# Optimization experiments

Hardware: AMD Instinct MI355X
Metric: run time of the kernel (lower is better)

## Reference

```python
import jax, jax.numpy as jnp
import numpy as np

DIM = 128
NUM_HEADS = 4
HEAD_DIM = DIM // NUM_HEADS
KSIZE = 7
DILATION = 1
SCALE = HEAD_DIM ** -0.5


def _rpb_bias(rpb):
    # Faithful to _get_rpb_indices: indices do NOT depend on query position.
    coords = np.stack(np.meshgrid(np.arange(KSIZE), np.arange(KSIZE), indexing='ij'))
    coords = coords.reshape(2, -1).T  # [K*K, 2]
    rel = coords - KSIZE // 2 + (KSIZE - 1)
    return rpb[:, rel[:, 0], rel[:, 1]]  # [NH, K*K]


def setup_inputs() -> dict:
    key = jax.random.key(0)
    ks = jax.random.split(key, 6)
    B, H, W = 4, 56, 56
    x = jax.random.normal(ks[0], (B, H, W, DIM), dtype=jnp.float32)
    qkv_w = jax.random.normal(ks[1], (3 * DIM, DIM), dtype=jnp.float32) * 0.02
    qkv_b = jnp.zeros((3 * DIM,), dtype=jnp.float32)
    rpb = jax.random.normal(ks[2], (NUM_HEADS, 2 * KSIZE - 1, 2 * KSIZE - 1), dtype=jnp.float32) * 0.02
    proj_w = jax.random.normal(ks[3], (DIM, DIM), dtype=jnp.float32) * 0.02
    proj_b = jnp.zeros((DIM,), dtype=jnp.float32)
    return {"x": x, "qkv_w": qkv_w, "qkv_b": qkv_b, "rpb": rpb, "proj_w": proj_w, "proj_b": proj_b}


def reference(x, qkv_w, qkv_b, rpb, proj_w, proj_b):
    B, H, W, C = x.shape
    qkv = x @ qkv_w.T + qkv_b                                   # [B,H,W,3C]
    qkv = qkv.reshape(B, H, W, 3, NUM_HEADS, HEAD_DIM).transpose(3, 0, 4, 1, 2, 5)
    q, k, v = qkv[0], qkv[1], qkv[2]                            # [B,NH,H,W,HD]

    pad = (KSIZE // 2) * DILATION
    # Zero padding — padded positions stay in the softmax (faithful, no masking).
    kp = jnp.pad(k, ((0, 0), (0, 0), (pad, pad), (pad, pad), (0, 0)))
    vp = jnp.pad(v, ((0, 0), (0, 0), (pad, pad), (pad, pad), (0, 0)))

    off = jnp.arange(0, KSIZE * DILATION, DILATION)
    idx_i = jnp.arange(H)[:, None] + off[None, :]               # [H,K]
    idx_j = jnp.arange(W)[:, None] + off[None, :]               # [W,K]
    Ai = idx_i[:, None, :, None]                                # [H,1,K,1]
    Aj = idx_j[None, :, None, :]                                # [1,W,1,K]
    k_win = kp[:, :, Ai, Aj, :].reshape(B, NUM_HEADS, H, W, KSIZE * KSIZE, HEAD_DIM)
    v_win = vp[:, :, Ai, Aj, :].reshape(B, NUM_HEADS, H, W, KSIZE * KSIZE, HEAD_DIM)

    bias = _rpb_bias(rpb)                                       # [NH, K*K]
    attn = jnp.einsum('bnhwd,bnhwkd->bnhwk', q, k_win) * SCALE
    attn = attn + bias[None, :, None, None, :]
    attn = jax.nn.softmax(attn, axis=-1)
    out = jnp.einsum('bnhwk,bnhwkd->bnhwd', attn, v_win)        # [B,NH,H,W,HD]
    out = out.transpose(0, 2, 3, 1, 4).reshape(B, H, W, C)
    return out @ proj_w.T + proj_b
```

## Files before the change

kernel.cpp:

```cpp
#include <hip/hip_runtime.h>

#define NPIX   3136
#define MROWS  12544
#define QKV_STRIDE 1605632
#define SCALE  0.17677669529663687f
#define KVS    136
#define HP     140

typedef __attribute__((ext_vector_type(8))) _Float16 half8;
typedef __attribute__((ext_vector_type(2))) _Float16 v2h;
typedef __attribute__((ext_vector_type(4))) float    f32x4;

#if defined(__has_builtin)
#if __has_builtin(__builtin_amdgcn_fdot2)
#define HAS_FDOT2 1
#endif
#endif

__device__ __forceinline__ float quad_reduce_sum(float x) {
    x += __int_as_float(__builtin_amdgcn_mov_dpp(__float_as_int(x), 0xB1, 0xF, 0xF, true));
    x += __int_as_float(__builtin_amdgcn_mov_dpp(__float_as_int(x), 0x4E, 0xF, 0xF, true));
    return x;
}

__device__ __forceinline__ float dot8h(half8 a, half8 b, float acc) {
#ifdef HAS_FDOT2
    union { half8 v; v2h p[4]; } ua, ub;
    ua.v = a; ub.v = b;
    acc = __builtin_amdgcn_fdot2(ua.p[0], ub.p[0], acc, false);
    acc = __builtin_amdgcn_fdot2(ua.p[1], ub.p[1], acc, false);
    acc = __builtin_amdgcn_fdot2(ua.p[2], ub.p[2], acc, false);
    acc = __builtin_amdgcn_fdot2(ua.p[3], ub.p[3], acc, false);
#else
#pragma unroll
    for (int i = 0; i < 8; ++i) acc += (float)a[i] * (float)b[i];
#endif
    return acc;
}

template<int BM, int BN, int WM, int WN>
__global__ __launch_bounds__(256)
void qkv_mfma(const float* __restrict__ A, const float* __restrict__ W,
              const float* __restrict__ bias, _Float16* __restrict__ outh,
              const float* __restrict__ pw, _Float16* __restrict__ pwh)
{
    constexpr int WTM = BM / WM;
    constexpr int WTN = BN / WN;
    constexpr int FM  = WTM / 16;
    constexpr int FN  = WTN / 16;
    constexpr int AIT = BM * 16 / 256;
    constexpr int WIT = BN * 16 / 256;
    const int row0 = blockIdx.x * BM;
    const int col0 = blockIdx.y * BN;
    const int t  = threadIdx.x;
    const int w  = t >> 6;
    const int l  = t & 63;
    const int wm = w / WN;
    const int wn = w % WN;

    if (blockIdx.y == 0 && blockIdx.x < 16) {
        int idx = blockIdx.x * 256 + t;
        float4 v = *reinterpret_cast<const float4*>(pw + (size_t)idx * 4);
        union { _Float16 h[4]; uint2 u; } cv;
        cv.h[0] = (_Float16)v.x; cv.h[1] = (_Float16)v.y;
        cv.h[2] = (_Float16)v.z; cv.h[3] = (_Float16)v.w;
        *reinterpret_cast<uint2*>(pwh + (size_t)idx * 4) = cv.u;
    }

    __shared__ _Float16 Ah[BM * 128];
    __shared__ _Float16 Wh[BN * 128];

    float4 pa[AIT], pwr[WIT];

#pragma unroll
    for (int it = 0; it < AIT; ++it) {
        int idx = t + it * 256;
        int r = idx >> 4, k0 = (idx & 15) << 2;
        pa[it] = *reinterpret_cast<const float4*>(A + (size_t)(row0 + r) * 128 + k0);
    }
#pragma unroll
    for (int it = 0; it < WIT; ++it) {
        int idx = t + it * 256;
        int r = idx >> 4, k0 = (idx & 15) << 2;
        pwr[it] = *reinterpret_cast<const float4*>(W + (size_t)(col0 + r) * 128 + k0);
    }
#pragma unroll
    for (int it = 0; it < AIT; ++it) {
        int idx = t + it * 256;
        int r = idx >> 4, k0 = (idx & 15) << 2;
        union { _Float16 h[4]; uint2 u; } cv;
        cv.h[0] = (_Float16)pa[it].x; cv.h[1] = (_Float16)pa[it].y;
        cv.h[2] = (_Float16)pa[it].z; cv.h[3] = (_Float16)pa[it].w;
        *reinterpret_cast<uint2*>(&Ah[r * 128 + (k0 ^ ((r & 7) << 3))]) = cv.u;
    }
#pragma unroll
    for (int it = 0; it < WIT; ++it) {
        int idx = t + it * 256;
        int r = idx >> 4, k0 = (idx & 15) << 2;
        union { _Float16 h[4]; uint2 u; } cv;
        cv.h[0] = (_Float16)pwr[it].x; cv.h[1] = (_Float16)pwr[it].y;
        cv.h[2] = (_Float16)pwr[it].z; cv.h[3] = (_Float16)pwr[it].w;
        *reinterpret_cast<uint2*>(&Wh[r * 128 + (k0 ^ ((r & 7) << 3))]) = cv.u;
    }
    __syncthreads();

#pragma unroll
    for (int it = 0; it < AIT; ++it) {
        int idx = t + it * 256;
        int r = idx >> 4, k0 = 64 + ((idx & 15) << 2);
        pa[it] = *reinterpret_cast<const float4*>(A + (size_t)(row0 + r) * 128 + k0);
    }
#pragma unroll
    for (int it = 0; it < WIT; ++it) {
        int idx = t + it * 256;
        int r = idx >> 4, k0 = 64 + ((idx & 15) << 2);
        pwr[it] = *reinterpret_cast<const float4*>(W + (size_t)(col0 + r) * 128 + k0);
    }

    f32x4 acc[FM][FN];
#pragma unroll
    for (int mf = 0; mf < FM; ++mf)
#pragma unroll
        for (int nf = 0; nf < FN; ++nf) acc[mf][nf] = (f32x4){0.f, 0.f, 0.f, 0.f};

#pragma unroll
    for (int ks = 0; ks < 2; ++ks) {
        const int kb = ks * 32 + ((l >> 4) << 3);
        half8 a[FM], b[FN];
#pragma unroll
        for (int mf = 0; mf < FM; ++mf) {
            int m = wm * WTM + mf * 16 + (l & 15);
            a[mf] = *reinterpret_cast<const half8*>(&Ah[m * 128 + (kb ^ ((m & 7) << 3))]);
        }
#pragma unroll
        for (int nf = 0; nf < FN; ++nf) {
            int n = wn * WTN + nf * 16 + (l & 15);
            b[nf] = *reinterpret_cast<const half8*>(&Wh[n * 128 + (kb ^ ((n & 7) << 3))]);
        }
#pragma unroll
        for (int mf = 0; mf < FM; ++mf)
#pragma unroll
            for (int nf = 0; nf < FN; ++nf)
                acc[mf][nf] = __builtin_amdgcn_mfma_f32_16x16x32_f16(
                    a[mf], b[nf], acc[mf][nf], 0, 0, 0);
    }

#pragma unroll
    for (int it = 0; it < AIT; ++it) {
        int idx = t + it * 256;
        int r = idx >> 4, k0 = 64 + ((idx & 15) << 2);
        union { _Float16 h[4]; uint2 u; } cv;
        cv.h[0] = (_Float16)pa[it].x; cv.h[1] = (_Float16)pa[it].y;
        cv.h[2] = (_Float16)pa[it].z; cv.h[3] = (_Float16)pa[it].w;
        *reinterpret_cast<uint2*>(&Ah[r * 128 + (k0 ^ ((r & 7) << 3))]) = cv.u;
    }
#pragma unroll
    for (int it = 0; it < WIT; ++it) {
        int idx = t + it * 256;
        int r = idx >> 4, k0 = 64 + ((idx & 15) << 2);
        union { _Float16 h[4]; uint2 u; } cv;
        cv.h[0] = (_Float16)pwr[it].x; cv.h[1] = (_Float16)pwr[it].y;
        cv.h[2] = (_Float16)pwr[it].z; cv.h[3] = (_Float16)pwr[it].w;
        *reinterpret_cast<uint2*>(&Wh[r * 128 + (k0 ^ ((r & 7) << 3))]) = cv.u;
    }
    __syncthreads();

#pragma unroll
    for (int ks = 2; ks < 4; ++ks) {
        const int kb = ks * 32 + ((l >> 4) << 3);
        half8 a[FM], b[FN];
#pragma unroll
        for (int mf = 0; mf < FM; ++mf) {
            int m = wm * WTM + mf * 16 + (l & 15);
            a[mf] = *reinterpret_cast<const half8*>(&Ah[m * 128 + (kb ^ ((m & 7) << 3))]);
        }
#pragma unroll
        for (int nf = 0; nf < FN; ++nf) {
            int n = wn * WTN + nf * 16 + (l & 15);
            b[nf] = *reinterpret_cast<const half8*>(&Wh[n * 128 + (kb ^ ((n & 7) << 3))]);
        }
#pragma unroll
        for (int mf = 0; mf < FM; ++mf)
#pragma unroll
            for (int nf = 0; nf < FN; ++nf)
                acc[mf][nf] = __builtin_amdgcn_mfma_f32_16x16x32_f16(
                    a[mf], b[nf], acc[mf][nf], 0, 0, 0);
    }

#pragma unroll
    for (int mf = 0; mf < FM; ++mf) {
#pragma unroll
        for (int nf = 0; nf < FN; ++nf) {
#pragma unroll
            for (int r = 0; r < 4; ++r) {
                int row = row0 + wm * WTM + mf * 16 + ((l >> 4) << 2) + r;
                int col = col0 + wn * WTN + nf * 16 + (l & 15);
                float val = acc[mf][nf][r] + bias[col];
                int b_  = row / NPIX;
                int pix = row - b_ * NPIX;
                int which = col >> 7;
                outh[(size_t)which * QKV_STRIDE +
                     ((size_t)b_ * NPIX + pix) * 128 + (col & 127)] = (_Float16)val;
            }
        }
    }
}

__global__ __launch_bounds__(512, 4)
void natten_proj_k(const _Float16* __restrict__ qb, const _Float16* __restrict__ kb,
                   const _Float16* __restrict__ vb, const float* __restrict__ rpb,
                   const _Float16* __restrict__ pwh, const float* __restrict__ pb,
                   float* __restrict__ out)
{
    extern __shared__ _Float16 smem[];
    _Float16* ksm  = smem;
    _Float16* vsm  = smem + HP * KVS;
    _Float16* atts = smem;

    const int flat = blockIdx.x;
    const int rank = (flat & 7) * 49 + (flat >> 3);
    const int tile = rank % 98;
    const int b    = rank / 98;
    const int ti = (tile / 14) * 8;
    const int tj = (tile % 14) * 4;
    const int t   = threadIdx.x;
    const int sub = t & 3;
    const int px  = (t >> 2) & 31;
    const int pi  = px >> 2;
    const int pj  = px & 3;
    const int h   = t >> 7;

    const _Float16* kbase = kb + (size_t)b * NPIX * 128;
    const _Float16* vbase = vb + (size_t)b * NPIX * 128;

    const int pix = (ti + pi) * 56 + (tj + pj);
    half8 qv = *reinterpret_cast<const half8*>(
        qb + ((size_t)b * NPIX + pix) * 128 + h * 32 + sub * 8);

    for (int e = t; e < HP * 16; e += 512) {
        int p = e >> 4, g = e & 15;
        int wi = p / 10, wj = p - wi * 10;
        int gi = ti - 3 + wi, gj = tj - 3 + wj;
        bool ok = ((unsigned)gi < 56u) && ((unsigned)gj < 56u);
        size_t src = ((size_t)(gi * 56 + gj)) * 128 + g * 8;
        half8 kv = (half8){0,0,0,0,0,0,0,0};
        if (ok) kv = *reinterpret_cast<const half8*>(kbase + src);
        *reinterpret_cast<half8*>(&ksm[p * KVS + g * 8]) = kv;
        half8 vv = (half8){0,0,0,0,0,0,0,0};
        if (ok) vv = *reinterpret_cast<const half8*>(vbase + src);
        *reinterpret_cast<half8*>(&vsm[p * KVS + g * 8]) = vv;
    }

    __syncthreads();

    const float* bias = rpb + h * 169;
    float logits[49];
    float m = -1e30f;
#pragma unroll
    for (int ki = 0; ki < 7; ++ki) {
#pragma unroll
        for (int kj = 0; kj < 7; ++kj) {
            int nb = (pi + ki) * 10 + (pj + kj);
            half8 kk = *reinterpret_cast<const half8*>(&ksm[nb * KVS + h * 32 + sub * 8]);
            float s = dot8h(qv, kk, 0.f);
            s = quad_reduce_sum(s);
            float lg = s * SCALE + bias[(ki + 3) * 13 + (kj + 3)];
            logits[ki * 7 + kj] = lg;
            m = fmaxf(m, lg);
        }
    }

    __syncthreads();

    float sum = 0.f;
#pragma unroll
    for (int n = 0; n < 49; ++n) {
        float e = __expf(logits[n] - m);
        logits[n] = e;
        sum += e;
    }
    float inv = 1.f / sum;

    float o[8] = {0.f, 0.f, 0.f, 0.f, 0.f, 0.f, 0.f, 0.f};
#pragma unroll
    for (int ki = 0; ki < 7; ++ki) {
#pragma unroll
        for (int kj = 0; kj < 7; ++kj) {
            int nb = (pi + ki) * 10 + (pj + kj);
            half8 vv = *reinterpret_cast<const half8*>(&vsm[nb * KVS + h * 32 + sub * 8]);
            float wgt = logits[ki * 7 + kj];
#pragma unroll
            for (int i = 0; i < 8; ++i)
                o[i] += wgt * (float)vv[i];
        }
    }

    const int l   = t & 63;
    const int wv  = t >> 6;
    const int wm  = wv & 1;
    const int wn  = wv >> 1;
    const int kb0 = (l >> 4) << 3;
    half8 wreg[8];
#pragma unroll
    for (int ks = 0; ks < 4; ++ks) {
        const _Float16* wp = pwh + (size_t)(wn * 32 + (l & 15)) * 128 + ks * 32 + kb0;
        wreg[ks]     = *reinterpret_cast<const half8*>(wp);
        wreg[4 + ks] = *reinterpret_cast<const half8*>(wp + 16 * 128);
    }

    {
        half8 r;
#pragma unroll
        for (int i = 0; i < 8; ++i) r[i] = (_Float16)(o[i] * inv);
        *reinterpret_cast<half8*>(&atts[px * KVS + h * 32 + sub * 8]) = r;
    }

    __syncthreads();

    f32x4 acc0 = (f32x4){0.f, 0.f, 0.f, 0.f};
    f32x4 acc1 = (f32x4){0.f, 0.f, 0.f, 0.f};
#pragma unroll
    for (int ks = 0; ks < 4; ++ks) {
        const int kb = ks * 32 + kb0;
        half8 a = *reinterpret_cast<const half8*>(&atts[(wm * 16 + (l & 15)) * KVS + kb]);
        acc0 = __builtin_amdgcn_mfma_f32_16x16x32_f16(a, wreg[ks],     acc0, 0, 0, 0);
        acc1 = __builtin_amdgcn_mfma_f32_16x16x32_f16(a, wreg[4 + ks], acc1, 0, 0, 0);
    }

#pragma unroll
    for (int r = 0; r < 4; ++r) {
        int prow = wm * 16 + ((l >> 4) << 2) + r;
        int gpix = (ti + (prow >> 2)) * 56 + tj + (prow & 3);
        float* dst = out + ((size_t)b * NPIX + gpix) * 128;
        int c0 = wn * 32 + (l & 15);
        dst[c0]      = acc0[r] + pb[c0];
        dst[c0 + 16] = acc1[r] + pb[c0 + 16];
    }
}

extern "C" void kernel_launch(void* const* d_in, const int* in_sizes, int n_in,
                              void* d_out, int out_size, void* d_ws, size_t ws_size,
                              hipStream_t stream)
{
    const float* x      = (const float*)d_in[0];
    const float* qkv_w  = (const float*)d_in[1];
    const float* qkv_b  = (const float*)d_in[2];
    const float* rpb    = (const float*)d_in[3];
    const float* proj_w = (const float*)d_in[4];
    const float* proj_b = (const float*)d_in[5];
    float* out = (float*)d_out;

    _Float16* qbuf = (_Float16*)d_ws;
    _Float16* kbuf = qbuf + (size_t)QKV_STRIDE;
    _Float16* vbuf = kbuf + (size_t)QKV_STRIDE;
    _Float16* pwh  = vbuf + (size_t)QKV_STRIDE;

    hipFuncSetAttribute((const void*)natten_proj_k,
                        hipFuncAttributeMaxDynamicSharedMemorySize,
                        2 * HP * KVS * (int)sizeof(_Float16));

    qkv_mfma<64, 128, 2, 2><<<dim3(196, 3), dim3(256), 0, stream>>>(
        x, qkv_w, qkv_b, qbuf, proj_w, pwh);

    natten_proj_k<<<dim3(392), dim3(512),
                    2 * HP * KVS * sizeof(_Float16), stream>>>(
        qbuf, kbuf, vbuf, rpb, pwh, proj_b, out);
}
```

Measured before the change: 30.41 us.

## Shrink attention tiles to 4x4 with XOR-swizzled K/V shared memory

The fused attention+projection kernel now processes 4x4 pixel tiles with 256 threads per block instead of 8x4 tiles with 512 threads, doubling the grid to 784 blocks. K/V shared-memory tiles shrink to a 10x10 halo and use an XOR swizzle instead of row padding to avoid bank conflicts, and the buffer becomes static. The aim is better load balance across CUs and lower LDS use per block. In exchange, halo overhead per output pixel grows (100 loaded neighbours for 16 pixels versus 140 for 32), which increases global K/V traffic.

```diff
diff --git a/kernel.cpp b/kernel.cpp
--- a/kernel.cpp
+++ b/kernel.cpp
@@ -4,8 +4,10 @@
 #define MROWS  12544
 #define QKV_STRIDE 1605632
 #define SCALE  0.17677669529663687f
-#define KVS    136
-#define HP     140
+#define ASTR   136
+#define HP2    100
+
+#define KVIDX(p, d) (((p) << 7) + ((d) ^ (((p) & 7) << 3)))
 
 typedef __attribute__((ext_vector_type(8))) _Float16 half8;
 typedef __attribute__((ext_vector_type(2))) _Float16 v2h;
@@ -206,29 +208,29 @@
     }
 }
 
-__global__ __launch_bounds__(512, 4)
+__global__ __launch_bounds__(256, 3)
 void natten_proj_k(const _Float16* __restrict__ qb, const _Float16* __restrict__ kb,
                    const _Float16* __restrict__ vb, const float* __restrict__ rpb,
                    const _Float16* __restrict__ pwh, const float* __restrict__ pb,
                    float* __restrict__ out)
 {
-    extern __shared__ _Float16 smem[];
+    __shared__ _Float16 smem[2 * HP2 * 128];
     _Float16* ksm  = smem;
-    _Float16* vsm  = smem + HP * KVS;
+    _Float16* vsm  = smem + HP2 * 128;
     _Float16* atts = smem;
 
     const int flat = blockIdx.x;
-    const int rank = (flat & 7) * 49 + (flat >> 3);
-    const int tile = rank % 98;
-    const int b    = rank / 98;
-    const int ti = (tile / 14) * 8;
+    const int rank = (flat & 7) * 98 + (flat >> 3);
+    const int tile = rank % 196;
+    const int b    = rank / 196;
+    const int ti = (tile / 14) * 4;
     const int tj = (tile % 14) * 4;
     const int t   = threadIdx.x;
     const int sub = t & 3;
-    const int px  = (t >> 2) & 31;
+    const int px  = (t >> 2) & 15;
     const int pi  = px >> 2;
     const int pj  = px & 3;
-    const int h   = t >> 7;
+    const int h   = t >> 6;
 
     const _Float16* kbase = kb + (size_t)b * NPIX * 128;
     const _Float16* vbase = vb + (size_t)b * NPIX * 128;
@@ -237,7 +239,7 @@
     half8 qv = *reinterpret_cast<const half8*>(
         qb + ((size_t)b * NPIX + pix) * 128 + h * 32 + sub * 8);
 
-    for (int e = t; e < HP * 16; e += 512) {
+    for (int e = t; e < HP2 * 16; e += 256) {
         int p = e >> 4, g = e & 15;
         int wi = p / 10, wj = p - wi * 10;
         int gi = ti - 3 + wi, gj = tj - 3 + wj;
@@ -245,15 +247,16 @@
         size_t src = ((size_t)(gi * 56 + gj)) * 128 + g * 8;
         half8 kv = (half8){0,0,0,0,0,0,0,0};
         if (ok) kv = *reinterpret_cast<const half8*>(kbase + src);
-        *reinterpret_cast<half8*>(&ksm[p * KVS + g * 8]) = kv;
+        *reinterpret_cast<half8*>(&ksm[KVIDX(p, g * 8)]) = kv;
         half8 vv = (half8){0,0,0,0,0,0,0,0};
         if (ok) vv = *reinterpret_cast<const half8*>(vbase + src);
-        *reinterpret_cast<half8*>(&vsm[p * KVS + g * 8]) = vv;
+        *reinterpret_cast<half8*>(&vsm[KVIDX(p, g * 8)]) = vv;
     }
 
     __syncthreads();
 
     const float* bias = rpb + h * 169;
+    const int dl = h * 32 + sub * 8;
     float logits[49];
     float m = -1e30f;
 #pragma unroll
@@ -261,7 +264,7 @@
 #pragma unroll
         for (int kj = 0; kj < 7; ++kj) {
             int nb = (pi + ki) * 10 + (pj + kj);
-            half8 kk = *reinterpret_cast<const half8*>(&ksm[nb * KVS + h * 32 + sub * 8]);
+            half8 kk = *reinterpret_cast<const half8*>(&ksm[KVIDX(nb, dl)]);
             float s = dot8h(qv, kk, 0.f);
             s = quad_reduce_sum(s);
             float lg = s * SCALE + bias[(ki + 3) * 13 + (kj + 3)];
@@ -287,7 +290,7 @@
 #pragma unroll
         for (int kj = 0; kj < 7; ++kj) {
             int nb = (pi + ki) * 10 + (pj + kj);
-            half8 vv = *reinterpret_cast<const half8*>(&vsm[nb * KVS + h * 32 + sub * 8]);
+            half8 vv = *reinterpret_cast<const half8*>(&vsm[KVIDX(nb, dl)]);
             float wgt = logits[ki * 7 + kj];
 #pragma unroll
             for (int i = 0; i < 8; ++i)
@@ -296,9 +299,7 @@
     }
 
     const int l   = t & 63;
-    const int wv  = t >> 6;
-    const int wm  = wv & 1;
-    const int wn  = wv >> 1;
+    const int wn  = t >> 6;
     const int kb0 = (l >> 4) << 3;
     half8 wreg[8];
 #pragma unroll
@@ -312,7 +313,7 @@
         half8 r;
 #pragma unroll
         for (int i = 0; i < 8; ++i) r[i] = (_Float16)(o[i] * inv);
-        *reinterpret_cast<half8*>(&atts[px * KVS + h * 32 + sub * 8]) = r;
+        *reinterpret_cast<half8*>(&atts[px * ASTR + h * 32 + sub * 8]) = r;
     }
 
     __syncthreads();
@@ -322,14 +323,14 @@
 #pragma unroll
     for (int ks = 0; ks < 4; ++ks) {
         const int kb = ks * 32 + kb0;
-        half8 a = *reinterpret_cast<const half8*>(&atts[(wm * 16 + (l & 15)) * KVS + kb]);
+        half8 a = *reinterpret_cast<const half8*>(&atts[(l & 15) * ASTR + kb]);
         acc0 = __builtin_amdgcn_mfma_f32_16x16x32_f16(a, wreg[ks],     acc0, 0, 0, 0);
         acc1 = __builtin_amdgcn_mfma_f32_16x16x32_f16(a, wreg[4 + ks], acc1, 0, 0, 0);
     }
 
 #pragma unroll
     for (int r = 0; r < 4; ++r) {
-        int prow = wm * 16 + ((l >> 4) << 2) + r;
+        int prow = ((l >> 4) << 2) + r;
         int gpix = (ti + (prow >> 2)) * 56 + tj + (prow & 3);
         float* dst = out + ((size_t)b * NPIX + gpix) * 128;
         int c0 = wn * 32 + (l & 15);
@@ -355,14 +356,9 @@
     _Float16* vbuf = kbuf + (size_t)QKV_STRIDE;
     _Float16* pwh  = vbuf + (size_t)QKV_STRIDE;
 
-    hipFuncSetAttribute((const void*)natten_proj_k,
-                        hipFuncAttributeMaxDynamicSharedMemorySize,
-                        2 * HP * KVS * (int)sizeof(_Float16));
-
     qkv_mfma<64, 128, 2, 2><<<dim3(196, 3), dim3(256), 0, stream>>>(
         x, qkv_w, qkv_b, qbuf, proj_w, pwh);
 
-    natten_proj_k<<<dim3(392), dim3(512),
-                    2 * HP * KVS * sizeof(_Float16), stream>>>(
+    natten_proj_k<<<dim3(784), dim3(256), 0, stream>>>(
         qbuf, kbuf, vbuf, rpb, pwh, proj_b, out);
 }
```

Result: slower. 34.53 us (+13.5%).
